# Kernel optimization log

Hardware: AMD Instinct MI355X
Metric: run time of the kernel (lower is better)

Reference implementation:

```python
import jax, jax.numpy as jnp
import numpy as np
import math

N = 2_000_000
NUM_LEVELS = 16
MIN_RES, MAX_RES = 16, 2048
FEAT = 2
GROWTH = math.exp((math.log(MAX_RES) - math.log(MIN_RES)) / (NUM_LEVELS - 1))
RES = np.array([int(MIN_RES * GROWTH ** i) for i in range(NUM_LEVELS)], dtype=np.int32)
# Source bug (replicated faithfully): hash is taken mod len(hash_tables[0].weight) = min(16**3, 2**19) = 4096 for ALL levels.
HASH_MOD = min(MIN_RES ** 3, 2 ** 19)  # 4096
PRIMES_MOD = np.array([1 % HASH_MOD, 2654435761 % HASH_MOD, 805459861 % HASH_MOD], dtype=np.int32)
HID, GEO, HIDC, APP = 64, 15, 64, 32


def _lin(key, fin, fout):
    k1, k2 = jax.random.split(key)
    return (jax.random.normal(k1, (fin, fout), jnp.float32) * 0.05,
            jax.random.normal(k2, (fout,), jnp.float32) * 0.01)


def setup_inputs() -> dict:
    key = jax.random.key(0)
    ks = jax.random.split(key, 16)
    inp = {}
    inp['ray_samples'] = jax.random.normal(ks[0], (N, 3), jnp.float32)
    inp['directions'] = jax.random.normal(ks[1], (N, 3), jnp.float32)
    inp['camera_indices'] = jax.random.randint(ks[2], (N,), 0, 1000, jnp.int32)
    inp['aabb'] = jnp.array([[-1.0, -1.0, -1.0], [1.0, 1.0, 1.0]], jnp.float32)
    # hash tables: only first HASH_MOD rows are reachable (source mod bug); init uniform(-1e-4, 1e-4)
    inp['hash_tables'] = jax.random.uniform(ks[3], (NUM_LEVELS, HASH_MOD, FEAT), jnp.float32, -1e-4, 1e-4)
    inp['dir_w1'], inp['dir_b1'] = _lin(ks[4], 3, 16)
    inp['dir_w2'], inp['dir_b2'] = _lin(ks[5], 16, 16)
    inp['dens_w1'], inp['dens_b1'] = _lin(ks[6], NUM_LEVELS * FEAT, HID)
    inp['dens_w2'], inp['dens_b2'] = _lin(ks[7], HID, HID)
    inp['dens_w3'], inp['dens_b3'] = _lin(ks[8], HID, 1 + GEO)
    cin = GEO + 16 + APP  # 63
    inp['col_w1'], inp['col_b1'] = _lin(ks[9], cin, HIDC)
    inp['col_w2'], inp['col_b2'] = _lin(ks[10], HIDC, HIDC)
    inp['col_w3'], inp['col_b3'] = _lin(ks[11], HIDC, 3)
    inp['app_emb'] = jax.random.normal(ks[12], (1000, APP), jnp.float32) * 0.01
    return inp


def hash_encode(positions, hash_tables):
    # positions: [N,3] in [0,1]; hash_tables: [L, HASH_MOD, FEAT]
    res = jnp.asarray(RES)  # [L]
    scaled = positions[None, :, :] * (res[:, None, None] - 1).astype(jnp.float32)  # [L,N,3]
    coords = jnp.clip(jnp.floor(scaled).astype(jnp.int32), 0, res[:, None, None] - 1)
    # (coords * primes).sum(-1) % HASH_MOD, computed mod-safe in int32
    h = (coords * jnp.asarray(PRIMES_MOD)).sum(-1) % HASH_MOD  # [L,N]
    feats = hash_tables[jnp.arange(NUM_LEVELS)[:, None], h]  # [L,N,FEAT] (no trilinear interp, per source)
    return jnp.transpose(feats, (1, 0, 2)).reshape(positions.shape[0], NUM_LEVELS * FEAT)  # [N,32]


def reference(ray_samples, directions, camera_indices, aabb, hash_tables,
              dir_w1, dir_b1, dir_w2, dir_b2,
              dens_w1, dens_b1, dens_w2, dens_b2, dens_w3, dens_b3,
              col_w1, col_b1, col_w2, col_b2, col_w3, col_b3, app_emb):
    positions = jnp.clip((ray_samples - aabb[0]) / (aabb[1] - aabb[0]), 0.0, 1.0)
    enc = hash_encode(positions, hash_tables)  # [N,32]
    h = jax.nn.relu(enc @ dens_w1 + dens_b1)
    h = jax.nn.relu(h @ dens_w2 + dens_b2)
    dfeat = h @ dens_w3 + dens_b3  # [N,16]
    density = jax.nn.relu(dfeat[:, :1])
    geo = dfeat[:, 1:]
    edir = jax.nn.relu(directions @ dir_w1 + dir_b1) @ dir_w2 + dir_b2  # [N,16]
    cin = jnp.concatenate([geo, edir, app_emb[camera_indices]], axis=-1)  # [N,63]
    c = jax.nn.relu(cin @ col_w1 + col_b1)
    c = jax.nn.relu(c @ col_w2 + col_b2)
    rgb = jax.nn.sigmoid(c @ col_w3 + col_b3)  # [N,3]
    return jnp.concatenate([rgb, density, geo], axis=-1)  # [N,19]
```

## Files before the change

kernel.cpp:

```cpp
#include <hip/hip_runtime.h>
#include <math.h>


typedef short short8 __attribute__((ext_vector_type(8)));
typedef float f32x4 __attribute__((ext_vector_type(4)));
typedef float f32x4a __attribute__((ext_vector_type(4), aligned(4)));
typedef float f32x2a __attribute__((ext_vector_type(2), aligned(4)));
typedef unsigned int uint;
typedef unsigned short ushort;

struct EncC { float rf[16]; };

#define PY 2481
#define PZ 1941

#define MFMA(A,B,C) __builtin_amdgcn_mfma_f32_16x16x32_bf16(A, B, C, 0, 0, 0)

#define W1_OFF   0
#define W3_OFF   5120
#define C3_OFF   7424
#define DB1_OFF  9728
#define DB2_OFF  9984
#define DB3_OFF  10240
#define CB1_OFF  10304
#define CB2_OFF  10560
#define CB3_OFF  10816
#define W2_OFF   10848
#define C1_OFF   20064
#define C2_OFF   29280
#define ACT_OFF  10848
#define LDS_BYTES 47712

__device__ __forceinline__ uint bf16rne(float x) {
    uint u = __builtin_bit_cast(uint, x);
    return (u + 0x7fffu + ((u >> 16) & 1u)) >> 16;
}
__device__ __forceinline__ uint pktr(float lo, float hi) {
    return __builtin_amdgcn_perm(__builtin_bit_cast(uint, hi),
                                 __builtin_bit_cast(uint, lo), 0x07060302u);
}

__device__ __forceinline__ void layer_wb(const f32x4* acc, char* rowp, int q) {
#pragma unroll
    for (int mt = 0; mt < 4; ++mt) {
        const f32x4 v = acc[mt];
        uint2 pw;
        pw.x = pktr(fmaxf(v[0], 0.f), fmaxf(v[1], 0.f));
        pw.y = pktr(fmaxf(v[2], 0.f), fmaxf(v[3], 0.f));
        *(uint2*)(rowp + mt*32 + q*8) = pw;
    }
}

__device__ __forceinline__ void layer64(char* wact, const short8* aw,
                                        const char* biasp, int l15, int q) {
    const int q16 = q * 16;
    f32x4 bf[4];
#pragma unroll
    for (int mt = 0; mt < 4; ++mt)
        bf[mt] = *(const f32x4*)(biasp + mt*64 + q16);
#pragma unroll
    for (int nt = 0; nt < 4; ++nt) {
        char* rowp = wact + (nt*16 + l15)*144;
        short8 b0 = *(const short8*)(rowp + q16);
        short8 b1 = *(const short8*)(rowp + 64 + q16);
        f32x4 acc[4];
#pragma unroll
        for (int mt = 0; mt < 4; ++mt) {
            f32x4 z = MFMA(aw[2*mt], b0, bf[mt]);
            acc[mt] = MFMA(aw[2*mt + 1], b1, z);
        }
        layer_wb(acc, rowp, q);
    }
}

__global__ __launch_bounds__(256, 3)
void nerf_mfma(const float* __restrict__ ray, const float* __restrict__ dirs,
               const int* __restrict__ cam_idx, const float* __restrict__ aabb,
               const float* __restrict__ ht,
               const float* __restrict__ dir_w1, const float* __restrict__ dir_b1,
               const float* __restrict__ dir_w2, const float* __restrict__ dir_b2,
               const float* __restrict__ dens_w1, const float* __restrict__ dens_b1,
               const float* __restrict__ dens_w2, const float* __restrict__ dens_b2,
               const float* __restrict__ dens_w3, const float* __restrict__ dens_b3,
               const float* __restrict__ col_w1, const float* __restrict__ col_b1,
               const float* __restrict__ col_w2, const float* __restrict__ col_b2,
               const float* __restrict__ col_w3, const float* __restrict__ col_b3,
               const float* __restrict__ app_emb,
               float* __restrict__ out, int n, EncC enc)
{
    __shared__ __align__(16) char smem[LDS_BYTES];
    const int t = threadIdx.x;

    {
        uint* z = (uint*)smem;
        for (int i = t; i < 38496/4; i += 256) z[i] = 0;
    }
    __syncthreads();
    {
        ushort* w1t = (ushort*)(smem + W1_OFF);
        for (int e = t; e < 2048; e += 256) w1t[(e&63)*40 + (e>>6)] = (ushort)bf16rne(dens_w1[e]);
        ushort* w2t = (ushort*)(smem + W2_OFF);
        for (int e = t; e < 4096; e += 256) w2t[(e&63)*72 + (e>>6)] = (ushort)bf16rne(dens_w2[e]);
        ushort* w3t = (ushort*)(smem + W3_OFF);
        for (int e = t; e < 1024; e += 256) w3t[(e&15)*72 + (e>>4)] = (ushort)bf16rne(dens_w3[e]);
        ushort* c1t = (ushort*)(smem + C1_OFF);
        for (int e = t; e < 4032; e += 256) {
            int in = e >> 6, o = e & 63;
            int pk = (in < 15) ? (in + 49) : ((in < 31) ? (in + 17) : (in - 31));
            c1t[o*72 + pk] = (ushort)bf16rne(col_w1[e]);
        }
        ushort* c2t = (ushort*)(smem + C2_OFF);
        for (int e = t; e < 4096; e += 256) c2t[(e&63)*72 + (e>>6)] = (ushort)bf16rne(col_w2[e]);
        ushort* c3t = (ushort*)(smem + C3_OFF);
        for (int e = t; e < 192; e += 256) c3t[(e%3)*72 + (e/3)] = (ushort)bf16rne(col_w3[e]);
        if (t < 64) {
            *(float*)(smem + DB1_OFF + t*4) = dens_b1[t];
            *(float*)(smem + DB2_OFF + t*4) = dens_b2[t];
            *(float*)(smem + CB1_OFF + t*4) = col_b1[t];
            *(float*)(smem + CB2_OFF + t*4) = col_b2[t];
        }
        if (t < 16) *(float*)(smem + DB3_OFF + t*4) = dens_b3[t];
        if (t < 4)  *(float*)(smem + CB3_OFF + t*4) = (t < 3) ? col_b3[t] : 0.f;
    }
    __syncthreads();

    const int w = t >> 6, lane = t & 63, l15 = lane & 15, q = lane >> 4;
    const int q16 = q * 16;
    char* wact = smem + ACT_OFF + w*9216;

    short8 aD2[8], aC1[8], aC2[8];
#pragma unroll
    for (int mt = 0; mt < 4; ++mt)
#pragma unroll
        for (int kk = 0; kk < 2; ++kk) {
            const int ro = (mt*16 + l15)*144 + kk*64 + q16;
            aD2[mt*2+kk] = *(const short8*)(smem + W2_OFF + ro);
            aC1[mt*2+kk] = *(const short8*)(smem + C1_OFF + ro);
            aC2[mt*2+kk] = *(const short8*)(smem + C2_OFF + ro);
        }
    __syncthreads();

    const float a0x = aabb[0], a0y = aabb[1], a0z = aabb[2];
    const float ivx = 1.f/(aabb[3]-a0x), ivy = 1.f/(aabb[4]-a0y), ivz = 1.f/(aabb[5]-a0z);

    const int ntiles = (n + 255) >> 8;
    for (int tile = blockIdx.x; tile < ntiles; tile += gridDim.x) {
        const int base = tile*256 + w*64;
        if (base >= n) continue;
        const bool full = (base + 64 <= n);
        const int sc = full ? (base + lane) : min(base + lane, n - 1);
        float* otile = out + (size_t)base * 19;

        float px = fminf(fmaxf((ray[3*sc  ] - a0x)*ivx, 0.f), 1.f);
        float py = fminf(fmaxf((ray[3*sc+1] - a0y)*ivy, 0.f), 1.f);
        float pz = fminf(fmaxf((ray[3*sc+2] - a0z)*ivz, 0.f), 1.f);
        uint encp[16];
#pragma unroll
        for (int l = 0; l < 16; ++l) {
            const float rf = enc.rf[l];
            const int cx = (int)(px*rf), cy = (int)(py*rf), cz = (int)(pz*rf);
            const int h = (cx + cy*PY + cz*PZ) & 4095;
            const float2 f = *(const float2*)(ht + (((l<<12) + h) << 1));
            encp[l] = pktr(f.x, f.y);
        }
        uint4* arow = (uint4*)(wact + lane*144);
        arow[0] = make_uint4(encp[0],  encp[1],  encp[2],  encp[3]);
        arow[1] = make_uint4(encp[4],  encp[5],  encp[6],  encp[7]);
        arow[2] = make_uint4(encp[8],  encp[9],  encp[10], encp[11]);
        arow[3] = make_uint4(encp[12], encp[13], encp[14], encp[15]);

        {
            short8 a1[4];
            f32x4 bf[4];
#pragma unroll
            for (int mt = 0; mt < 4; ++mt) {
                a1[mt] = *(const short8*)(smem + W1_OFF + (mt*16 + l15)*80 + q16);
                bf[mt] = *(const f32x4*)(smem + DB1_OFF + mt*64 + q16);
            }
#pragma unroll
            for (int nt = 0; nt < 4; ++nt) {
                char* rowp = wact + (nt*16 + l15)*144;
                short8 b = *(const short8*)(rowp + q16);
                f32x4 acc[4];
#pragma unroll
                for (int mt = 0; mt < 4; ++mt)
                    acc[mt] = MFMA(a1[mt], b, bf[mt]);
                layer_wb(acc, rowp, q);
            }
        }
        layer64(wact, aD2, smem + DB2_OFF, l15, q);
        {
            short8 a0 = *(const short8*)(smem + W3_OFF + l15*144 + q16);
            short8 a1 = *(const short8*)(smem + W3_OFF + l15*144 + 64 + q16);
            f32x4 bb3 = *(const f32x4*)(smem + DB3_OFF + q16);
#pragma unroll
            for (int nt = 0; nt < 4; ++nt) {
                char* rowp = wact + (nt*16 + l15)*144;
                short8 b0 = *(const short8*)(rowp + q16);
                short8 b1 = *(const short8*)(rowp + 64 + q16);
                f32x4 z = MFMA(a0, b0, bb3);
                f32x4 v = MFMA(a1, b1, z);
                uint2 g;
                g.x = pktr(q == 0 ? 0.f : v[0], v[1]);
                g.y = pktr(v[2], v[3]);
                *(uint2*)(rowp + 96 + 8*q) = g;
                if (q == 0) v[0] = fmaxf(v[0], 0.f);
                const int sg = nt*16 + l15;
                if (full || base + sg < n)
                    *(f32x4a*)(otile + sg*19 + 3 + q16/4) = v;
            }
        }
        {
            const float dx = dirs[3*sc], dy = dirs[3*sc+1], dz = dirs[3*sc+2];
            float e1[16];
#pragma unroll
            for (int j = 0; j < 16; ++j)
                e1[j] = fmaxf(fmaf(dx, dir_w1[j],
                              fmaf(dy, dir_w1[16+j],
                              fmaf(dz, dir_w1[32+j], dir_b1[j]))), 0.f);
            float ed[16];
#pragma unroll
            for (int j = 0; j < 16; ++j) ed[j] = dir_b2[j];
#pragma unroll
            for (int i = 0; i < 16; ++i) {
                const float e = e1[i];
#pragma unroll
                for (int j = 0; j < 16; ++j) ed[j] = fmaf(e, dir_w2[i*16+j], ed[j]);
            }
            const int cam = cam_idx[sc];
            const float4* ap = (const float4*)(app_emb + (size_t)cam*32);
            uint pk[16];
#pragma unroll
            for (int qd = 0; qd < 8; ++qd) {
                const float4 vv = ap[qd];
                pk[2*qd]   = pktr(vv.x, vv.y);
                pk[2*qd+1] = pktr(vv.z, vv.w);
            }
            arow[0] = make_uint4(pk[0],  pk[1],  pk[2],  pk[3]);
            arow[1] = make_uint4(pk[4],  pk[5],  pk[6],  pk[7]);
            arow[2] = make_uint4(pk[8],  pk[9],  pk[10], pk[11]);
            arow[3] = make_uint4(pk[12], pk[13], pk[14], pk[15]);
            uint ep[8];
#pragma unroll
            for (int j = 0; j < 8; ++j) ep[j] = pktr(ed[2*j], ed[2*j+1]);
            arow[4] = make_uint4(ep[0], ep[1], ep[2], ep[3]);
            arow[5] = make_uint4(ep[4], ep[5], ep[6], ep[7]);
        }
        layer64(wact, aC1, smem + CB1_OFF, l15, q);
        layer64(wact, aC2, smem + CB2_OFF, l15, q);
        {
            short8 a0 = *(const short8*)(smem + C3_OFF + l15*144 + q16);
            short8 a1 = *(const short8*)(smem + C3_OFF + l15*144 + 64 + q16);
            f32x4 bbc = *(const f32x4*)(smem + CB3_OFF);
#pragma unroll
            for (int nt = 0; nt < 4; ++nt) {
                char* rowp = wact + (nt*16 + l15)*144;
                short8 b0 = *(const short8*)(rowp + q16);
                short8 b1 = *(const short8*)(rowp + 64 + q16);
                f32x4 z = MFMA(a0, b0, bbc);
                f32x4 v = MFMA(a1, b1, z);
                const int sg = nt*16 + l15;
                if (q == 0 && (full || base + sg < n)) {
                    float* op = otile + sg*19;
                    f32x2a r01;
                    r01[0] = 1.f / (1.f + __expf(-v[0]));
                    r01[1] = 1.f / (1.f + __expf(-v[1]));
                    *(f32x2a*)op = r01;
                    op[2] = 1.f / (1.f + __expf(-v[2]));
                }
            }
        }
    }
}

extern "C" void kernel_launch(void* const* d_in, const int* in_sizes, int n_in,
                              void* d_out, int out_size, void* d_ws, size_t ws_size,
                              hipStream_t stream)
{
    const float* ray  = (const float*)d_in[0];
    const float* dirs = (const float*)d_in[1];
    const int*   cam  = (const int*)  d_in[2];
    const float* aabb = (const float*)d_in[3];
    const float* ht   = (const float*)d_in[4];
    const float* dw1  = (const float*)d_in[5];
    const float* db1  = (const float*)d_in[6];
    const float* dw2  = (const float*)d_in[7];
    const float* db2  = (const float*)d_in[8];
    const float* nw1  = (const float*)d_in[9];
    const float* nb1  = (const float*)d_in[10];
    const float* nw2  = (const float*)d_in[11];
    const float* nb2  = (const float*)d_in[12];
    const float* nw3  = (const float*)d_in[13];
    const float* nb3  = (const float*)d_in[14];
    const float* cw1  = (const float*)d_in[15];
    const float* cb1  = (const float*)d_in[16];
    const float* cw2  = (const float*)d_in[17];
    const float* cb2  = (const float*)d_in[18];
    const float* cw3  = (const float*)d_in[19];
    const float* cb3  = (const float*)d_in[20];
    const float* app  = (const float*)d_in[21];
    float* out = (float*)d_out;

    const int n = in_sizes[0] / 3;

    EncC enc;
    const double growth = exp((log(2048.0) - log(16.0)) / 15.0);
    for (int i = 0; i < 16; ++i) {
        const int r = (int)(16.0 * pow(growth, (double)i));
        enc.rf[i] = (float)(r - 1);
    }

    const int ntiles = (n + 255) / 256;
    const int grid = ntiles < 768 ? ntiles : 768;
    nerf_mfma<<<grid, 256, 0, stream>>>(
        ray, dirs, cam, aabb, ht,
        dw1, db1, dw2, db2,
        nw1, nb1, nw2, nb2, nw3, nb3,
        cw1, cb1, cw2, cb2, cw3, cb3,
        app, out, n, enc);
}
```

Measured before the change: 418.7 us.

## XOR-swizzle LDS layouts, shrink LDS footprint, and raise occupancy to four blocks

Replaces the padded 144-byte-stride LDS rows for activations and weights with 128-byte rows using an XOR swizzle on 16-byte chunks, so MFMA operand reads avoid bank conflicts without padding. The staged weights now share the activation region, and the dens_w3 and col_w3 fragments are preloaded into registers. This cuts LDS use enough to allow four blocks per CU, so launch bounds and the persistent grid go up. The cost is more register pressure from the extra fragments under the tighter launch bound, and the swizzled index arithmetic has to stay consistent across every layer.

```diff
diff --git a/kernel.cpp b/kernel.cpp
--- a/kernel.cpp
+++ b/kernel.cpp
@@ -17,19 +17,19 @@
 #define MFMA(A,B,C) __builtin_amdgcn_mfma_f32_16x16x32_bf16(A, B, C, 0, 0, 0)
 
 #define W1_OFF   0
-#define W3_OFF   5120
-#define C3_OFF   7424
-#define DB1_OFF  9728
-#define DB2_OFF  9984
-#define DB3_OFF  10240
-#define CB1_OFF  10304
-#define CB2_OFF  10560
-#define CB3_OFF  10816
-#define W2_OFF   10848
-#define C1_OFF   20064
-#define C2_OFF   29280
-#define ACT_OFF  10848
-#define LDS_BYTES 47712
+#define DB1_OFF  4096
+#define DB2_OFF  4352
+#define DB3_OFF  4608
+#define CB1_OFF  4672
+#define CB2_OFF  4928
+#define CB3_OFF  5184
+#define ACT_OFF  5248
+#define LDS_BYTES 38016
+#define SW2_OFF  (ACT_OFF)
+#define SC1_OFF  (ACT_OFF + 8192)
+#define SC2_OFF  (ACT_OFF + 16384)
+#define SW3_OFF  (ACT_OFF + 24576)
+#define SC3_OFF  (ACT_OFF + 26624)
 
 __device__ __forceinline__ uint bf16rne(float x) {
     uint u = __builtin_bit_cast(uint, x);
@@ -40,40 +40,42 @@
                                  __builtin_bit_cast(uint, lo), 0x07060302u);
 }
 
-__device__ __forceinline__ void layer_wb(const f32x4* acc, char* rowp, int q) {
+__device__ __forceinline__ void layer_wb(const f32x4* acc, char* rowp, int q, int s7) {
+    const int lo = (q & 1) * 8, qh = q >> 1;
 #pragma unroll
     for (int mt = 0; mt < 4; ++mt) {
         const f32x4 v = acc[mt];
         uint2 pw;
         pw.x = pktr(fmaxf(v[0], 0.f), fmaxf(v[1], 0.f));
         pw.y = pktr(fmaxf(v[2], 0.f), fmaxf(v[3], 0.f));
-        *(uint2*)(rowp + mt*32 + q*8) = pw;
+        *(uint2*)(rowp + ((((2*mt + qh) ^ s7) << 4) | lo)) = pw;
     }
 }
 
 __device__ __forceinline__ void layer64(char* wact, const short8* aw,
-                                        const char* biasp, int l15, int q) {
+                                        const char* biasp, int l15, int q, int s7) {
     const int q16 = q * 16;
     f32x4 bf[4];
 #pragma unroll
     for (int mt = 0; mt < 4; ++mt)
         bf[mt] = *(const f32x4*)(biasp + mt*64 + q16);
+    const int o0 = ((q ^ s7) << 4), o1 = (((4 | q) ^ s7) << 4);
 #pragma unroll
     for (int nt = 0; nt < 4; ++nt) {
-        char* rowp = wact + (nt*16 + l15)*144;
-        short8 b0 = *(const short8*)(rowp + q16);
-        short8 b1 = *(const short8*)(rowp + 64 + q16);
+        char* rowp = wact + (nt*16 + l15)*128;
+        short8 b0 = *(const short8*)(rowp + o0);
+        short8 b1 = *(const short8*)(rowp + o1);
         f32x4 acc[4];
 #pragma unroll
         for (int mt = 0; mt < 4; ++mt) {
             f32x4 z = MFMA(aw[2*mt], b0, bf[mt]);
             acc[mt] = MFMA(aw[2*mt + 1], b1, z);
         }
-        layer_wb(acc, rowp, q);
-    }
-}
-
-__global__ __launch_bounds__(256, 3)
+        layer_wb(acc, rowp, q, s7);
+    }
+}
+
+__global__ __launch_bounds__(256, 4)
 void nerf_mfma(const float* __restrict__ ray, const float* __restrict__ dirs,
                const int* __restrict__ cam_idx, const float* __restrict__ aabb,
                const float* __restrict__ ht,
@@ -88,31 +90,44 @@
                const float* __restrict__ app_emb,
                float* __restrict__ out, int n, EncC enc)
 {
-    __shared__ __align__(16) char smem[LDS_BYTES];
+    __shared__ __align__(128) char smem[LDS_BYTES];
     const int t = threadIdx.x;
 
     {
-        uint* z = (uint*)smem;
-        for (int i = t; i < 38496/4; i += 256) z[i] = 0;
-    }
-    __syncthreads();
-    {
-        ushort* w1t = (ushort*)(smem + W1_OFF);
-        for (int e = t; e < 2048; e += 256) w1t[(e&63)*40 + (e>>6)] = (ushort)bf16rne(dens_w1[e]);
-        ushort* w2t = (ushort*)(smem + W2_OFF);
-        for (int e = t; e < 4096; e += 256) w2t[(e&63)*72 + (e>>6)] = (ushort)bf16rne(dens_w2[e]);
-        ushort* w3t = (ushort*)(smem + W3_OFF);
-        for (int e = t; e < 1024; e += 256) w3t[(e&15)*72 + (e>>4)] = (ushort)bf16rne(dens_w3[e]);
-        ushort* c1t = (ushort*)(smem + C1_OFF);
+        for (int e = t; e < 2048; e += 256) {
+            const int in = e >> 6, o = e & 63;
+            const int b = o*64 + ((((in>>3) ^ (o&3)) << 4) | ((in&7)*2));
+            *(ushort*)(smem + W1_OFF + b) = (ushort)bf16rne(dens_w1[e]);
+        }
+        for (int e = t; e < 4096; e += 256) {
+            const int in = e >> 6, o = e & 63;
+            const int sw = (((in>>3) ^ (o&7)) << 4) | ((in&7)*2);
+            *(ushort*)(smem + SW2_OFF + o*128 + sw) = (ushort)bf16rne(dens_w2[e]);
+        }
         for (int e = t; e < 4032; e += 256) {
-            int in = e >> 6, o = e & 63;
-            int pk = (in < 15) ? (in + 49) : ((in < 31) ? (in + 17) : (in - 31));
-            c1t[o*72 + pk] = (ushort)bf16rne(col_w1[e]);
-        }
-        ushort* c2t = (ushort*)(smem + C2_OFF);
-        for (int e = t; e < 4096; e += 256) c2t[(e&63)*72 + (e>>6)] = (ushort)bf16rne(col_w2[e]);
-        ushort* c3t = (ushort*)(smem + C3_OFF);
-        for (int e = t; e < 192; e += 256) c3t[(e%3)*72 + (e/3)] = (ushort)bf16rne(col_w3[e]);
+            const int in = e >> 6, o = e & 63;
+            const int pk = (in < 15) ? (in + 49) : ((in < 31) ? (in + 17) : (in - 31));
+            const int sw = (((pk>>3) ^ (o&7)) << 4) | ((pk&7)*2);
+            *(ushort*)(smem + SC1_OFF + o*128 + sw) = (ushort)bf16rne(col_w1[e]);
+        }
+        if (t < 64) {
+            *(ushort*)(smem + SC1_OFF + t*128 + ((6 ^ (t&7)) << 4)) = 0;
+        }
+        for (int e = t; e < 4096; e += 256) {
+            const int in = e >> 6, o = e & 63;
+            const int sw = (((in>>3) ^ (o&7)) << 4) | ((in&7)*2);
+            *(ushort*)(smem + SC2_OFF + o*128 + sw) = (ushort)bf16rne(col_w2[e]);
+        }
+        for (int e = t; e < 1024; e += 256) {
+            const int in = e >> 4, o = e & 15;
+            const int sw = (((in>>3) ^ (o&7)) << 4) | ((in&7)*2);
+            *(ushort*)(smem + SW3_OFF + o*128 + sw) = (ushort)bf16rne(dens_w3[e]);
+        }
+        for (int e = t; e < 192; e += 256) {
+            const int o = e % 3, in = e / 3;
+            const int sw = (((in>>3) ^ (o&7)) << 4) | ((in&7)*2);
+            *(ushort*)(smem + SC3_OFF + o*128 + sw) = (ushort)bf16rne(col_w3[e]);
+        }
         if (t < 64) {
             *(float*)(smem + DB1_OFF + t*4) = dens_b1[t];
             *(float*)(smem + DB2_OFF + t*4) = dens_b2[t];
@@ -125,19 +140,27 @@
     __syncthreads();
 
     const int w = t >> 6, lane = t & 63, l15 = lane & 15, q = lane >> 4;
-    const int q16 = q * 16;
-    char* wact = smem + ACT_OFF + w*9216;
-
-    short8 aD2[8], aC1[8], aC2[8];
+    const int q16 = q * 16, s7 = lane & 7;
+    char* wact = smem + ACT_OFF + w*8192;
+
+    short8 aD2[8], aC1[8], aC2[8], aW3[2], aC3[2];
 #pragma unroll
     for (int mt = 0; mt < 4; ++mt)
 #pragma unroll
         for (int kk = 0; kk < 2; ++kk) {
-            const int ro = (mt*16 + l15)*144 + kk*64 + q16;
-            aD2[mt*2+kk] = *(const short8*)(smem + W2_OFF + ro);
-            aC1[mt*2+kk] = *(const short8*)(smem + C1_OFF + ro);
-            aC2[mt*2+kk] = *(const short8*)(smem + C2_OFF + ro);
-        }
+            const int ro = (mt*16 + l15)*128 + (((kk*4 + q) ^ s7) << 4);
+            aD2[mt*2+kk] = *(const short8*)(smem + SW2_OFF + ro);
+            aC1[mt*2+kk] = *(const short8*)(smem + SC1_OFF + ro);
+            aC2[mt*2+kk] = *(const short8*)(smem + SC2_OFF + ro);
+        }
+    {
+        const int r0 = l15*128 + ((q ^ s7) << 4);
+        const int r1 = l15*128 + (((4 | q) ^ s7) << 4);
+        aW3[0] = *(const short8*)(smem + SW3_OFF + r0);
+        aW3[1] = *(const short8*)(smem + SW3_OFF + r1);
+        aC3[0] = *(const short8*)(smem + SC3_OFF + r0);
+        aC3[1] = *(const short8*)(smem + SC3_OFF + r1);
+    }
     __syncthreads();
 
     const float a0x = aabb[0], a0y = aabb[1], a0z = aabb[2];
@@ -163,47 +186,51 @@
             const float2 f = *(const float2*)(ht + (((l<<12) + h) << 1));
             encp[l] = pktr(f.x, f.y);
         }
-        uint4* arow = (uint4*)(wact + lane*144);
-        arow[0] = make_uint4(encp[0],  encp[1],  encp[2],  encp[3]);
-        arow[1] = make_uint4(encp[4],  encp[5],  encp[6],  encp[7]);
-        arow[2] = make_uint4(encp[8],  encp[9],  encp[10], encp[11]);
-        arow[3] = make_uint4(encp[12], encp[13], encp[14], encp[15]);
-
-        {
+        {
+            char* wr = wact + lane*128;
+            *(uint4*)(wr + ((0 ^ s7) << 4)) = make_uint4(encp[0],  encp[1],  encp[2],  encp[3]);
+            *(uint4*)(wr + ((1 ^ s7) << 4)) = make_uint4(encp[4],  encp[5],  encp[6],  encp[7]);
+            *(uint4*)(wr + ((2 ^ s7) << 4)) = make_uint4(encp[8],  encp[9],  encp[10], encp[11]);
+            *(uint4*)(wr + ((3 ^ s7) << 4)) = make_uint4(encp[12], encp[13], encp[14], encp[15]);
+        }
+
+        {
+            const int s3 = lane & 3;
             short8 a1[4];
             f32x4 bf[4];
 #pragma unroll
             for (int mt = 0; mt < 4; ++mt) {
-                a1[mt] = *(const short8*)(smem + W1_OFF + (mt*16 + l15)*80 + q16);
+                a1[mt] = *(const short8*)(smem + W1_OFF + (mt*16 + l15)*64 + ((q ^ s3) << 4));
                 bf[mt] = *(const f32x4*)(smem + DB1_OFF + mt*64 + q16);
             }
+            const int o0 = ((q ^ s7) << 4);
 #pragma unroll
             for (int nt = 0; nt < 4; ++nt) {
-                char* rowp = wact + (nt*16 + l15)*144;
-                short8 b = *(const short8*)(rowp + q16);
+                char* rowp = wact + (nt*16 + l15)*128;
+                short8 b = *(const short8*)(rowp + o0);
                 f32x4 acc[4];
 #pragma unroll
                 for (int mt = 0; mt < 4; ++mt)
                     acc[mt] = MFMA(a1[mt], b, bf[mt]);
-                layer_wb(acc, rowp, q);
-            }
-        }
-        layer64(wact, aD2, smem + DB2_OFF, l15, q);
-        {
-            short8 a0 = *(const short8*)(smem + W3_OFF + l15*144 + q16);
-            short8 a1 = *(const short8*)(smem + W3_OFF + l15*144 + 64 + q16);
+                layer_wb(acc, rowp, q, s7);
+            }
+        }
+        layer64(wact, aD2, smem + DB2_OFF, l15, q, s7);
+        {
             f32x4 bb3 = *(const f32x4*)(smem + DB3_OFF + q16);
+            const int o0 = ((q ^ s7) << 4), o1 = (((4 | q) ^ s7) << 4);
+            const int og = ((((6 | (q >> 1)) ^ s7) << 4) | ((q & 1) * 8));
 #pragma unroll
             for (int nt = 0; nt < 4; ++nt) {
-                char* rowp = wact + (nt*16 + l15)*144;
-                short8 b0 = *(const short8*)(rowp + q16);
-                short8 b1 = *(const short8*)(rowp + 64 + q16);
-                f32x4 z = MFMA(a0, b0, bb3);
-                f32x4 v = MFMA(a1, b1, z);
+                char* rowp = wact + (nt*16 + l15)*128;
+                short8 b0 = *(const short8*)(rowp + o0);
+                short8 b1 = *(const short8*)(rowp + o1);
+                f32x4 z = MFMA(aW3[0], b0, bb3);
+                f32x4 v = MFMA(aW3[1], b1, z);
                 uint2 g;
                 g.x = pktr(q == 0 ? 0.f : v[0], v[1]);
                 g.y = pktr(v[2], v[3]);
-                *(uint2*)(rowp + 96 + 8*q) = g;
+                *(uint2*)(rowp + og) = g;
                 if (q == 0) v[0] = fmaxf(v[0], 0.f);
                 const int sg = nt*16 + l15;
                 if (full || base + sg < n)
@@ -236,29 +263,29 @@
                 pk[2*qd]   = pktr(vv.x, vv.y);
                 pk[2*qd+1] = pktr(vv.z, vv.w);
             }
-            arow[0] = make_uint4(pk[0],  pk[1],  pk[2],  pk[3]);
-            arow[1] = make_uint4(pk[4],  pk[5],  pk[6],  pk[7]);
-            arow[2] = make_uint4(pk[8],  pk[9],  pk[10], pk[11]);
-            arow[3] = make_uint4(pk[12], pk[13], pk[14], pk[15]);
+            char* wr = wact + lane*128;
+            *(uint4*)(wr + ((0 ^ s7) << 4)) = make_uint4(pk[0],  pk[1],  pk[2],  pk[3]);
+            *(uint4*)(wr + ((1 ^ s7) << 4)) = make_uint4(pk[4],  pk[5],  pk[6],  pk[7]);
+            *(uint4*)(wr + ((2 ^ s7) << 4)) = make_uint4(pk[8],  pk[9],  pk[10], pk[11]);
+            *(uint4*)(wr + ((3 ^ s7) << 4)) = make_uint4(pk[12], pk[13], pk[14], pk[15]);
             uint ep[8];
 #pragma unroll
             for (int j = 0; j < 8; ++j) ep[j] = pktr(ed[2*j], ed[2*j+1]);
-            arow[4] = make_uint4(ep[0], ep[1], ep[2], ep[3]);
-            arow[5] = make_uint4(ep[4], ep[5], ep[6], ep[7]);
-        }
-        layer64(wact, aC1, smem + CB1_OFF, l15, q);
-        layer64(wact, aC2, smem + CB2_OFF, l15, q);
-        {
-            short8 a0 = *(const short8*)(smem + C3_OFF + l15*144 + q16);
-            short8 a1 = *(const short8*)(smem + C3_OFF + l15*144 + 64 + q16);
+            *(uint4*)(wr + ((4 ^ s7) << 4)) = make_uint4(ep[0], ep[1], ep[2], ep[3]);
+            *(uint4*)(wr + ((5 ^ s7) << 4)) = make_uint4(ep[4], ep[5], ep[6], ep[7]);
+        }
+        layer64(wact, aC1, smem + CB1_OFF, l15, q, s7);
+        layer64(wact, aC2, smem + CB2_OFF, l15, q, s7);
+        {
             f32x4 bbc = *(const f32x4*)(smem + CB3_OFF);
+            const int o0 = ((q ^ s7) << 4), o1 = (((4 | q) ^ s7) << 4);
 #pragma unroll
             for (int nt = 0; nt < 4; ++nt) {
-                char* rowp = wact + (nt*16 + l15)*144;
-                short8 b0 = *(const short8*)(rowp + q16);
-                short8 b1 = *(const short8*)(rowp + 64 + q16);
-                f32x4 z = MFMA(a0, b0, bbc);
-                f32x4 v = MFMA(a1, b1, z);
+                char* rowp = wact + (nt*16 + l15)*128;
+                short8 b0 = *(const short8*)(rowp + o0);
+                short8 b1 = *(const short8*)(rowp + o1);
+                f32x4 z = MFMA(aC3[0], b0, bbc);
+                f32x4 v = MFMA(aC3[1], b1, z);
                 const int sg = nt*16 + l15;
                 if (q == 0 && (full || base + sg < n)) {
                     float* op = otile + sg*19;
@@ -311,7 +338,7 @@
     }
 
     const int ntiles = (n + 255) / 256;
-    const int grid = ntiles < 768 ? ntiles : 768;
+    const int grid = ntiles < 1024 ? ntiles : 1024;
     nerf_mfma<<<grid, 256, 0, stream>>>(
         ray, dirs, cam, aabb, ht,
         dw1, db1, dw2, db2,
```

New measurement: 578.0 us. 1.38x slower.
